# Optimization experiments

Hardware: AMD Instinct MI355X
Metric: run time of the kernel (lower is better)

Reference implementation:

```python
import jax, jax.numpy as jnp
import numpy as np

N = 262144
LOC_ENC_LEN = 60
NUM_WEIGHTS = 8
INDIM = 32
OUTDIM = 32
HIDDEN = 32
NEG_SLOPE = 0.01  # nn.LeakyReLU default


def _linear_init(key, fan_in, fan_out):
    # torch nn.Linear default: U(-1/sqrt(fan_in), 1/sqrt(fan_in))
    kw, kb = jax.random.split(key)
    bound = 1.0 / np.sqrt(fan_in)
    w = jax.random.uniform(kw, (fan_in, fan_out), jnp.float32, -bound, bound)
    b = jax.random.uniform(kb, (fan_out,), jnp.float32, -bound, bound)
    return w, b


def setup_inputs() -> dict:
    key = jax.random.key(0)
    ks = jax.random.split(key, 10)
    rel_loc_feat = jax.random.normal(ks[0], (N, LOC_ENC_LEN), jnp.float32)
    feat = jax.random.normal(ks[1], (N, INDIM), jnp.float32)
    dims = [LOC_ENC_LEN, HIDDEN, HIDDEN, HIDDEN, HIDDEN, HIDDEN, NUM_WEIGHTS]
    params = {}
    for i in range(6):
        w, b = _linear_init(ks[2 + i], dims[i], dims[i + 1])
        params[f'sn_w{i}'] = w
        params[f'sn_b{i}'] = b
    # weights_bank: kaiming_normal on [num_weights, indim*outdim] -> std = sqrt(2/fan_in), fan_in = indim*outdim
    std = np.sqrt(2.0 / (INDIM * OUTDIM))
    params['bank'] = jax.random.normal(ks[9], (NUM_WEIGHTS, INDIM * OUTDIM), jnp.float32) * std
    return {'rel_loc_feat': rel_loc_feat, 'feat': feat, **params}


def _score_net(x, ws, bs):
    # 5 Linear+LeakyReLU blocks, then final Linear (no activation)
    for i in range(5):
        x = x @ ws[i] + bs[i]
        x = jnp.where(x >= 0, x, NEG_SLOPE * x)
    return x @ ws[5] + bs[5]


def reference(rel_loc_feat, feat,
              sn_w0, sn_b0, sn_w1, sn_b1, sn_w2, sn_b2,
              sn_w3, sn_b3, sn_w4, sn_b4, sn_w5, sn_b5, bank):
    ws = [sn_w0, sn_w1, sn_w2, sn_w3, sn_w4, sn_w5]
    bs = [sn_b0, sn_b1, sn_b2, sn_b3, sn_b4, sn_b5]
    logits = _score_net(rel_loc_feat, ws, bs)          # [N, num_weights]
    coeff = jax.nn.softmax(logits, axis=-1)            # [N, num_weights]
    # per-point weight matrix: [N, indim*outdim] -> [N, indim, outdim]
    weights = (coeff @ bank).reshape(coeff.shape[0], INDIM, OUTDIM)
    # per-point matmul: feat[:, None] @ weights -> squeeze
    out = jnp.einsum('ni,nio->no', feat, weights)      # [N, outdim]
    return out
```

## Files before the change

kernel.cpp:

```cpp
#include <hip/hip_runtime.h>
#include <stdint.h>


typedef __attribute__((ext_vector_type(8))) __bf16 bf16x8;
typedef __attribute__((ext_vector_type(2))) __bf16 bf16x2;
typedef __attribute__((ext_vector_type(4))) float f32x4;

union FragU { uint32_t u[4]; bf16x8 v; uint4 q; };

__device__ __forceinline__ unsigned short f2bf(float f) {
    union { float f; uint32_t i; } v; v.f = f;
    return (unsigned short)((v.i + 0x7FFFu + ((v.i >> 16) & 1u)) >> 16);
}
__device__ __forceinline__ float bf2f(uint32_t u16) {
    union { uint32_t i; float f; } v; v.i = u16 << 16; return v.f;
}
__device__ __forceinline__ uint32_t pk2(float x, float y) {
    union { bf16x2 h; uint32_t u; } c;
    c.h[0] = (__bf16)x; c.h[1] = (__bf16)y;
    return c.u;
}
__device__ __forceinline__ bf16x8 pack8(float a, float b, float c, float d,
                                        float e, float f, float g, float h) {
    bf16x8 v;
    v[0] = (__bf16)a; v[1] = (__bf16)b; v[2] = (__bf16)c; v[3] = (__bf16)d;
    v[4] = (__bf16)e; v[5] = (__bf16)f; v[6] = (__bf16)g; v[7] = (__bf16)h;
    return v;
}
__device__ __forceinline__ int permK(int k) {
    return 4 * (k >> 3) + (k & 3) + 16 * ((k >> 2) & 1);
}
__device__ __forceinline__ f32x4 MF(bf16x8 a, bf16x8 b, f32x4 c) {
    return __builtin_amdgcn_mfma_f32_16x16x32_bf16(a, b, c, 0, 0, 0);
}


struct WPf { const float* p[13]; };

__global__ void pc_prep(WPf wp, uint32_t* __restrict__ ws) {
    int idx = blockIdx.x * blockDim.x + threadIdx.x;
    if (idx >= 10240) return;
    if (idx < 7424) {
        int layer, t, chunk = 0, lane, d; const float* w; bool perm;
        int r = idx;
        if (r < 1024) { chunk = r >> 9; r &= 511; t = r >> 8; r &= 255; lane = r >> 2; d = r & 3;
                        layer = 0; w = wp.p[0]; perm = false; }
        else if (r < 3072) { r -= 1024; layer = 1 + (r >> 9); r &= 511; t = r >> 8; r &= 255;
                             lane = r >> 2; d = r & 3; w = wp.p[2 * layer]; perm = true; }
        else if (r < 3328) { r -= 3072; layer = 5; t = 0; lane = r >> 2; d = r & 3;
                             w = wp.p[10]; perm = true; }
        else { r -= 3328; int bk = r >> 9; r &= 511; t = r >> 8; r &= 255; lane = r >> 2; d = r & 3;
               layer = -1; w = wp.p[12] + bk * 1024; perm = false; }
        int gq = lane >> 4, m = t * 16 + (lane & 15);
        uint32_t o = 0;
        #pragma unroll
        for (int e = 0; e < 2; ++e) {
            int kf = 8 * gq + 2 * d + e;
            float v = 0.f;
            if (layer == -1) {
                v = w[kf * 32 + m];
            } else {
                int ks = perm ? permK(kf) : (chunk * 32 + kf);
                if (layer == 0)      { if (ks < 60) v = w[ks * 32 + m]; }
                else if (layer == 5) { if (m < 8)   v = w[ks * 8 + m]; }
                else                 v = w[ks * 32 + m];
            }
            o |= ((uint32_t)f2bf(v)) << (16 * e);
        }
        ws[idx] = o;
    } else if (idx < 9984) {
        int r = idx - 7424; int L = r >> 9; r &= 511; int t = r >> 8; r &= 255;
        int lane = r >> 2, rr = r & 3;
        ((float*)ws)[idx] = wp.p[2 * L + 1][t * 16 + 4 * (lane >> 4) + rr];
    } else {
        int r = idx - 9984; int lane = r >> 2, rr = r & 3;
        int m = 4 * (lane >> 4) + rr;
        ((float*)ws)[idx] = (m < 8) ? wp.p[11][m] : 0.f;
    }
}

#define IT 2

__global__ __launch_bounds__(256) void pc_mlp(
    const float* __restrict__ rel, const uint32_t* __restrict__ wsu,
    uint32_t* __restrict__ outc)
{
    __shared__ __align__(16) uint32_t W[6144];
    {
        uint4* s4 = (uint4*)W;
        const uint4* g4 = (const uint4*)wsu;
        #pragma unroll
        for (int i = 0; i < 6; ++i) {
            int idx = threadIdx.x + 256 * i;
            s4[idx] = g4[idx < 832 ? idx : idx + 1024];
        }
    }
    __syncthreads();

    const int lane = threadIdx.x & 63;
    const int wv = threadIdx.x >> 6;
    const int g = lane >> 4;
    const int n16 = lane & 15;
    const size_t pt0 = (size_t)(blockIdx.x * 4 + wv) * (32 * IT);

    #define LDF(off) ({ FragU _f; _f.q = ((const uint4*)(W + (off)))[lane]; _f.v; })
    #define LDB(off) ({ float4 _b = ((const float4*)(W + (off)))[lane]; \
                        (f32x4){_b.x, _b.y, _b.z, _b.w}; })

    for (int it = 0; it < IT; ++it) {
        const size_t nA = pt0 + (size_t)it * 32 + n16;

        bf16x8 c0[2], c1[2];
        #pragma unroll
        for (int q = 0; q < 2; ++q) {
            const float* rrow = rel + (nA + 16 * q) * 60;
            float4 ra = *(const float4*)(rrow + 8 * g);
            float4 rb = *(const float4*)(rrow + 8 * g + 4);
            float4 rc = *(const float4*)(rrow + 32 + 8 * g);
            float4 rd = make_float4(0.f, 0.f, 0.f, 0.f);
            if (g < 3) rd = *(const float4*)(rrow + 36 + 8 * g);
            c0[q] = pack8(ra.x, ra.y, ra.z, ra.w, rb.x, rb.y, rb.z, rb.w);
            c1[q] = pack8(rc.x, rc.y, rc.z, rc.w, rd.x, rd.y, rd.z, rd.w);
        }

        f32x4 t0[2], t1[2];
        {
            f32x4 ba = LDB(3328), bb = LDB(3328 + 256);
            bf16x8 w00 = LDF(0), w01 = LDF(256), w10 = LDF(512), w11 = LDF(768);
            #pragma unroll
            for (int q = 0; q < 2; ++q) {
                t0[q] = MF(w00, c0[q], ba); t1[q] = MF(w01, c0[q], bb);
                t0[q] = MF(w10, c1[q], t0[q]); t1[q] = MF(w11, c1[q], t1[q]);
            }
        }

        #pragma unroll
        for (int L = 0; L < 4; ++L) {
            bf16x8 wa = LDF(1024 + L * 512), wb = LDF(1024 + L * 512 + 256);
            f32x4 ba = LDB(3328 + (L + 1) * 512), bb = LDB(3328 + (L + 1) * 512 + 256);
            #pragma unroll
            for (int q = 0; q < 2; ++q) {
                #pragma unroll
                for (int r = 0; r < 4; ++r) {
                    t0[q][r] = fmaxf(t0[q][r], 0.01f * t0[q][r]);
                    t1[q][r] = fmaxf(t1[q][r], 0.01f * t1[q][r]);
                }
                bf16x8 bx = pack8(t0[q][0], t0[q][1], t0[q][2], t0[q][3],
                                  t1[q][0], t1[q][1], t1[q][2], t1[q][3]);
                t0[q] = MF(wa, bx, ba);
                t1[q] = MF(wb, bx, bb);
            }
        }

        {
            bf16x8 w5 = LDF(3072);
            f32x4 b5 = LDB(5888);
            #pragma unroll
            for (int q = 0; q < 2; ++q) {
                #pragma unroll
                for (int r = 0; r < 4; ++r) {
                    t0[q][r] = fmaxf(t0[q][r], 0.01f * t0[q][r]);
                    t1[q][r] = fmaxf(t1[q][r], 0.01f * t1[q][r]);
                }
                bf16x8 bx = pack8(t0[q][0], t0[q][1], t0[q][2], t0[q][3],
                                  t1[q][0], t1[q][1], t1[q][2], t1[q][3]);
                t0[q] = MF(w5, bx, b5);
            }
        }

        #pragma unroll
        for (int q = 0; q < 2; ++q) {
            float m4 = fmaxf(fmaxf(t0[q][0], t0[q][1]), fmaxf(t0[q][2], t0[q][3]));
            float m8 = fmaxf(m4, __shfl_xor(m4, 16, 64));
            float e0 = __expf(t0[q][0] - m8), e1 = __expf(t0[q][1] - m8);
            float e2 = __expf(t0[q][2] - m8), e3 = __expf(t0[q][3] - m8);
            float s4 = e0 + e1 + e2 + e3;
            float s8 = s4 + __shfl_xor(s4, 16, 64);
            float inv = 1.0f / s8;
            uint32_t p01 = pk2(e0 * inv, e1 * inv);
            uint32_t p23 = pk2(e2 * inv, e3 * inv);
            if (g < 2)
                *(uint2*)(outc + (nA + 16 * q) * 32 + 2 * g) = make_uint2(p01, p23);
        }
    }
    #undef LDF
    #undef LDB
}

__global__ __launch_bounds__(256) void pc_bank(
    const float* __restrict__ feat, const uint32_t* __restrict__ wsu,
    float* out)
{
    __shared__ __align__(16) uint32_t W[4096];
    {
        uint4* s4 = (uint4*)W;
        const uint4* g4 = (const uint4*)wsu + 832;
        #pragma unroll
        for (int i = 0; i < 4; ++i) s4[threadIdx.x + 256 * i] = g4[threadIdx.x + 256 * i];
    }
    __syncthreads();

    const uint32_t* outc = (const uint32_t*)out;
    const int lane = threadIdx.x & 63;
    const int wv = threadIdx.x >> 6;
    const int g = lane >> 4;
    const int n16 = lane & 15;
    const size_t pt0 = (size_t)(blockIdx.x * 4 + wv) * (32 * IT);

    #define LDF(off) ({ FragU _f; _f.q = ((const uint4*)(W + (off)))[lane]; _f.v; })

    for (int it = 0; it < IT; ++it) {
        const size_t nA = pt0 + (size_t)it * 32 + n16;

        uint4 cp[2];
        #pragma unroll
        for (int q = 0; q < 2; ++q)
            cp[q] = *(const uint4*)(outc + (nA + 16 * q) * 32);

        bf16x8 bfr[2];
        #pragma unroll
        for (int q = 0; q < 2; ++q) {
            const float* frow = feat + (nA + 16 * q) * 32 + 8 * g;
            float4 fa = *(const float4*)frow;
            float4 fb = *(const float4*)(frow + 4);
            bfr[q] = pack8(fa.x, fa.y, fa.z, fa.w, fb.x, fb.y, fb.z, fb.w);
        }

        float cw[2][8];
        #pragma unroll
        for (int q = 0; q < 2; ++q) {
            cw[q][0] = bf2f(cp[q].x & 0xffff); cw[q][1] = bf2f(cp[q].x >> 16);
            cw[q][2] = bf2f(cp[q].y & 0xffff); cw[q][3] = bf2f(cp[q].y >> 16);
            cw[q][4] = bf2f(cp[q].z & 0xffff); cw[q][5] = bf2f(cp[q].z >> 16);
            cw[q][6] = bf2f(cp[q].w & 0xffff); cw[q][7] = bf2f(cp[q].w >> 16);
        }

        f32x4 o0[2], o1[2];
        #pragma unroll
        for (int q = 0; q < 2; ++q) {
            o0[q] = (f32x4){0.f, 0.f, 0.f, 0.f};
            o1[q] = (f32x4){0.f, 0.f, 0.f, 0.f};
        }
        #pragma unroll
        for (int k = 0; k < 8; ++k) {
            bf16x8 wk0 = LDF(k * 512), wk1 = LDF(k * 512 + 256);
            #pragma unroll
            for (int q = 0; q < 2; ++q) {
                f32x4 z = {0.f, 0.f, 0.f, 0.f};
                f32x4 u0 = MF(wk0, bfr[q], z);
                f32x4 u1 = MF(wk1, bfr[q], z);
                #pragma unroll
                for (int r = 0; r < 4; ++r) {
                    o0[q][r] += cw[q][k] * u0[r];
                    o1[q][r] += cw[q][k] * u1[r];
                }
            }
        }

        #pragma unroll
        for (int q = 0; q < 2; ++q) {
            float* orow = out + (nA + 16 * q) * 32;
            *(float4*)(orow + 4 * g)      = make_float4(o0[q][0], o0[q][1], o0[q][2], o0[q][3]);
            *(float4*)(orow + 16 + 4 * g) = make_float4(o1[q][0], o1[q][1], o1[q][2], o1[q][3]);
        }
    }
    #undef LDF
}

extern "C" void kernel_launch(void* const* d_in, const int* in_sizes, int n_in,
                              void* d_out, int out_size, void* d_ws, size_t ws_size,
                              hipStream_t stream)
{
    const float* rel = (const float*)d_in[0];
    const float* feat = (const float*)d_in[1];
    WPf wp;
    for (int i = 0; i < 13; ++i) wp.p[i] = (const float*)d_in[2 + i];
    uint32_t* ws = (uint32_t*)d_ws;
    float* out = (float*)d_out;

    const int npts = in_sizes[0] / 60;
    const int nblocks = npts / (32 * IT * 4);

    hipLaunchKernelGGL(pc_prep, dim3(40), dim3(256), 0, stream, wp, ws);
    hipLaunchKernelGGL(pc_mlp, dim3(nblocks), dim3(256), 0, stream, rel, ws, (uint32_t*)out);
    hipLaunchKernelGGL(pc_bank, dim3(nblocks), dim3(256), 0, stream, feat, ws, out);
}
```

Before: 180.5 us.

## Fuse score MLP and bank kernels, keep softmax coefficients in LDS

Merges the score-network kernel and the weight-bank kernel into one launch. The per-point softmax coefficients now go to shared memory instead of a global scratch area reused in the output buffer. This removes a kernel launch and the global write and read of the coefficients. In exchange shared memory per block grows to about 45 KB, which may cap occupancy, and the launch bounds now request 3 blocks per CU.

```diff
diff --git a/kernel.cpp b/kernel.cpp
--- a/kernel.cpp
+++ b/kernel.cpp
@@ -81,18 +81,23 @@
 
 #define IT 2
 
-__global__ __launch_bounds__(256) void pc_mlp(
-    const float* __restrict__ rel, const uint32_t* __restrict__ wsu,
-    uint32_t* __restrict__ outc)
+#define CO 10240
+
+__global__ __launch_bounds__(256, 3) void pc_main(
+    const float* __restrict__ rel, const float* __restrict__ feat,
+    const uint32_t* __restrict__ wsu, float* __restrict__ out)
 {
-    __shared__ __align__(16) uint32_t W[6144];
+    __shared__ __align__(16) uint32_t W[11264];
     {
         uint4* s4 = (uint4*)W;
         const uint4* g4 = (const uint4*)wsu;
         #pragma unroll
-        for (int i = 0; i < 6; ++i) {
+        for (int i = 0; i < 10; ++i) {
             int idx = threadIdx.x + 256 * i;
-            s4[idx] = g4[idx < 832 ? idx : idx + 1024];
+            int src = (idx < 832) ? idx
+                    : (idx < 1536) ? idx + 1024
+                    : idx - 704;
+            s4[idx] = g4[src];
         }
     }
     __syncthreads();
@@ -102,6 +107,7 @@
     const int g = lane >> 4;
     const int n16 = lane & 15;
     const size_t pt0 = (size_t)(blockIdx.x * 4 + wv) * (32 * IT);
+    const int pbase = wv * (32 * IT);
 
     #define LDF(off) ({ FragU _f; _f.q = ((const uint4*)(W + (off)))[lane]; _f.v; })
     #define LDB(off) ({ float4 _b = ((const float4*)(W + (off)))[lane]; \
@@ -129,7 +135,7 @@
             bf16x8 w00 = LDF(0), w01 = LDF(256), w10 = LDF(512), w11 = LDF(768);
             #pragma unroll
             for (int q = 0; q < 2; ++q) {
-                t0[q] = MF(w00, c0[q], ba); t1[q] = MF(w01, c0[q], bb);
+                t0[q] = MF(w00, c0[q], ba);    t1[q] = MF(w01, c0[q], bb);
                 t0[q] = MF(w10, c1[q], t0[q]); t1[q] = MF(w11, c1[q], t1[q]);
             }
         }
@@ -179,43 +185,21 @@
             float inv = 1.0f / s8;
             uint32_t p01 = pk2(e0 * inv, e1 * inv);
             uint32_t p23 = pk2(e2 * inv, e3 * inv);
-            if (g < 2)
-                *(uint2*)(outc + (nA + 16 * q) * 32 + 2 * g) = make_uint2(p01, p23);
-        }
-    }
-    #undef LDF
-    #undef LDB
-}
-
-__global__ __launch_bounds__(256) void pc_bank(
-    const float* __restrict__ feat, const uint32_t* __restrict__ wsu,
-    float* out)
-{
-    __shared__ __align__(16) uint32_t W[4096];
-    {
-        uint4* s4 = (uint4*)W;
-        const uint4* g4 = (const uint4*)wsu + 832;
-        #pragma unroll
-        for (int i = 0; i < 4; ++i) s4[threadIdx.x + 256 * i] = g4[threadIdx.x + 256 * i];
-    }
-    __syncthreads();
-
-    const uint32_t* outc = (const uint32_t*)out;
-    const int lane = threadIdx.x & 63;
-    const int wv = threadIdx.x >> 6;
-    const int g = lane >> 4;
-    const int n16 = lane & 15;
-    const size_t pt0 = (size_t)(blockIdx.x * 4 + wv) * (32 * IT);
-
-    #define LDF(off) ({ FragU _f; _f.q = ((const uint4*)(W + (off)))[lane]; _f.v; })
+            if (g < 2) {
+                int p = pbase + it * 32 + q * 16 + n16;
+                *(uint2*)(W + CO + p * 4 + 2 * g) = make_uint2(p01, p23);
+            }
+        }
+    }
 
     for (int it = 0; it < IT; ++it) {
         const size_t nA = pt0 + (size_t)it * 32 + n16;
+        const int p0 = pbase + it * 32 + n16;
 
         uint4 cp[2];
         #pragma unroll
         for (int q = 0; q < 2; ++q)
-            cp[q] = *(const uint4*)(outc + (nA + 16 * q) * 32);
+            cp[q] = *(const uint4*)(W + CO + (p0 + 16 * q) * 4);
 
         bf16x8 bfr[2];
         #pragma unroll
@@ -243,7 +227,7 @@
         }
         #pragma unroll
         for (int k = 0; k < 8; ++k) {
-            bf16x8 wk0 = LDF(k * 512), wk1 = LDF(k * 512 + 256);
+            bf16x8 wk0 = LDF(6144 + k * 512), wk1 = LDF(6144 + k * 512 + 256);
             #pragma unroll
             for (int q = 0; q < 2; ++q) {
                 f32x4 z = {0.f, 0.f, 0.f, 0.f};
@@ -265,6 +249,7 @@
         }
     }
     #undef LDF
+    #undef LDB
 }
 
 extern "C" void kernel_launch(void* const* d_in, const int* in_sizes, int n_in,
@@ -282,6 +267,5 @@
     const int nblocks = npts / (32 * IT * 4);
 
     hipLaunchKernelGGL(pc_prep, dim3(40), dim3(256), 0, stream, wp, ws);
-    hipLaunchKernelGGL(pc_mlp, dim3(nblocks), dim3(256), 0, stream, rel, ws, (uint32_t*)out);
-    hipLaunchKernelGGL(pc_bank, dim3(nblocks), dim3(256), 0, stream, feat, ws, out);
-}
+    hipLaunchKernelGGL(pc_main, dim3(nblocks), dim3(256), 0, stream, rel, feat, ws, out);
+}
```

Result: faster. 161.5 us (-10.5%).
